# Kernel tuning notes

Measured on AMD Instinct MI355X. Metric: run time of the kernel, lower is better.

Reference implementation:

```python
import math
import jax, jax.numpy as jnp
import numpy as np

B, S, D_MODEL, H = 2, 2048, 1024, 16
HEAD_DIM = D_MODEL // H
NUM_BUCKETS = 32
MAX_DISTANCE = 128
SCALING = HEAD_DIM ** (-0.5)


def setup_inputs() -> dict:
    key = jax.random.key(0)
    ks = jax.random.split(key, 6)
    inp = {
        "hidden_states": jax.random.normal(ks[0], (B, S, D_MODEL), jnp.float32),
        "Wq": jax.random.normal(ks[1], (D_MODEL, D_MODEL), jnp.float32) * (D_MODEL ** -0.5),
        "Wk": jax.random.normal(ks[2], (D_MODEL, D_MODEL), jnp.float32) * (D_MODEL ** -0.5),
        "Wv": jax.random.normal(ks[3], (D_MODEL, D_MODEL), jnp.float32) * (D_MODEL ** -0.5),
        "Wo": jax.random.normal(ks[4], (D_MODEL, D_MODEL), jnp.float32) * (D_MODEL ** -0.5),
        "rel_emb": jax.random.normal(ks[5], (NUM_BUCKETS, H), jnp.float32),
    }
    return inp


def _relative_position_bucket(relative_position, num_buckets=NUM_BUCKETS, max_distance=MAX_DISTANCE):
    # bidirectional (encoder) bucketing, matches T5 _relative_position_bucket
    num_buckets = num_buckets // 2
    relative_buckets = (relative_position > 0).astype(jnp.int32) * num_buckets
    relative_position = jnp.abs(relative_position)
    max_exact = num_buckets // 2
    is_small = relative_position < max_exact
    rp_f = jnp.maximum(relative_position, 1).astype(jnp.float32)  # guard log(0)
    rel_if_large = max_exact + (
        jnp.log(rp_f / max_exact) / math.log(max_distance / max_exact) * (num_buckets - max_exact)
    ).astype(jnp.int32)
    rel_if_large = jnp.minimum(rel_if_large, num_buckets - 1)
    relative_buckets = relative_buckets + jnp.where(is_small, relative_position, rel_if_large)
    return relative_buckets


def compute_bias(rel_emb, q_len, k_len):
    context_position = jnp.arange(q_len)[:, None]
    memory_position = jnp.arange(k_len)[None, :]
    relative_position = memory_position - context_position  # [q, k]
    buckets = _relative_position_bucket(relative_position)
    values = rel_emb[buckets]                  # [q, k, H]
    return jnp.transpose(values, (2, 0, 1))[None]  # [1, H, q, k]


def reference(hidden_states, Wq, Wk, Wv, Wo, rel_emb):
    b, s, _ = hidden_states.shape

    def shape(x):  # [b, s, d_model] -> [b, H, s, head_dim]
        return x.reshape(b, s, H, HEAD_DIM).transpose(0, 2, 1, 3)

    q = shape(hidden_states @ Wq.T)
    k = shape(hidden_states @ Wk.T)
    v = shape(hidden_states @ Wv.T)

    position_bias = compute_bias(rel_emb, s, s)            # [1, H, s, s]
    scores = jnp.einsum("bhqd,bhkd->bhqk", q, k) * SCALING + position_bias
    attn = jax.nn.softmax(scores, axis=-1)
    ctx = jnp.einsum("bhqk,bhkd->bhqd", attn, v)           # [b, H, s, head_dim]
    ctx = ctx.transpose(0, 2, 1, 3).reshape(b, s, D_MODEL)
    return ctx @ Wo.T
```

## Files before the change

### kernel.cpp

```cpp
#include <hip/hip_runtime.h>
#include <math.h>

#define H_    16
#define S_    2048
#define DH_   64
#define DM_   1024
#define NTOK_ 4096
#define NBIAS_ 4095

typedef __attribute__((ext_vector_type(8))) short short8;
typedef __attribute__((ext_vector_type(4))) float f32x4;

#define MFMA16(a, b, c) __builtin_amdgcn_mfma_f32_16x16x32_bf16((a), (b), (c), 0, 0, 0)

__device__ __forceinline__ ushort f2bf(float f) {
  union { float f; unsigned u; } x; x.f = f;
  unsigned r = (x.u + 0x7FFFu + ((x.u >> 16) & 1u)) >> 16;
  return (ushort)r;
}
__device__ __forceinline__ ushort f2bf_fast(float f) {
  union { float f; unsigned u; } x; x.f = f;
  return (ushort)((x.u + 0x8000u) >> 16);
}

__device__ __forceinline__ void ldg16_lds(const ushort* g, ushort* l) {
  __builtin_amdgcn_global_load_lds(
      (const __attribute__((address_space(1))) unsigned int*)g,
      (__attribute__((address_space(3))) unsigned int*)l, 16, 0, 0);
}

__global__ void cast_all_k(const float* __restrict__ hs,
                           const float* __restrict__ wq, const float* __restrict__ wk,
                           const float* __restrict__ wv, const float* __restrict__ wo,
                           ushort* __restrict__ out) {
  int i = (blockIdx.x * blockDim.x + threadIdx.x) * 4;
  const float* src;
  int off;
  if (i < NTOK_ * DM_) {
    src = hs; off = i;
  } else {
    int j = i - NTOK_ * DM_;
    int w = j >> 20;
    off = j & ((DM_ * DM_) - 1);
    src = (w == 0) ? wq : (w == 1) ? wk : (w == 2) ? wv : wo;
  }
  const float4 v = *(const float4*)(src + off);
  ushort4 o;
  o.x = f2bf(v.x); o.y = f2bf(v.y); o.z = f2bf(v.z); o.w = f2bf(v.w);
  *(ushort4*)(out + i) = o;
}

__global__ void build_bias_k(const float* __restrict__ rel_emb, float* __restrict__ biasTab) {
  int d = blockIdx.x * blockDim.x + threadIdx.x;
  if (d >= NBIAS_) return;
  int rp = d - (S_ - 1);
  int ret = (rp > 0) ? 16 : 0;
  int arp = rp < 0 ? -rp : rp;
  int bucket;
  if (arp < 8) {
    bucket = ret + arp;
  } else {
    float t = logf((float)arp * 0.125f);
    t = t / 2.772588722239781f;
    t = t * 8.0f;
    int large = 8 + (int)t;
    if (large > 15) large = 15;
    bucket = ret + large;
  }
  for (int h = 0; h < H_; ++h)
    biasTab[h * NBIAS_ + d] = rel_emb[bucket * H_ + h] * 1.4426950408889634f;
}

__global__ __launch_bounds__(256) void gemm_qkv_k(
    const ushort* __restrict__ X,
    const ushort* __restrict__ Wq, const ushort* __restrict__ Wk, const ushort* __restrict__ Wv,
    ushort* __restrict__ Q, ushort* __restrict__ K, ushort* __restrict__ Vt)
{
  const int z = blockIdx.z;
  const ushort* __restrict__ W = (z == 0) ? Wq : (z == 1) ? Wk : Wv;
  __shared__ __align__(16) ushort As[128 * 32];
  __shared__ __align__(16) ushort Bs[128 * 32];

  const int tid = threadIdx.x;
  const int wave = tid >> 6, lane = tid & 63;
  const int l15 = lane & 15, l4 = lane >> 4;
  const int wm = wave >> 1, wn = wave & 1;
  const int m0 = blockIdx.y * 128;
  const int n0 = blockIdx.x * 128;
  const int srow = lane >> 2, scol = (lane & 3) * 8;

  f32x4 acc[4][4];
#pragma unroll
  for (int mi = 0; mi < 4; ++mi)
#pragma unroll
    for (int ni = 0; ni < 4; ++ni) acc[mi][ni] = (f32x4){0.f, 0.f, 0.f, 0.f};

  for (int k0 = 0; k0 < DM_; k0 += 32) {
    __syncthreads();
#pragma unroll
    for (int i = 0; i < 4; ++i) {
      int c = wave * 4 + i;
      if (c < 8)
        ldg16_lds(X + (size_t)(m0 + c * 16 + srow) * DM_ + k0 + scol, &As[c * 512]);
      else
        ldg16_lds(W + (size_t)(n0 + (c - 8) * 16 + srow) * DM_ + k0 + scol, &Bs[(c - 8) * 512]);
    }
    __syncthreads();
    short8 af[4], bfr[4];
#pragma unroll
    for (int mi = 0; mi < 4; ++mi)
      af[mi] = *(const short8*)&As[(wm * 64 + mi * 16 + l15) * 32 + l4 * 8];
#pragma unroll
    for (int ni = 0; ni < 4; ++ni)
      bfr[ni] = *(const short8*)&Bs[(wn * 64 + ni * 16 + l15) * 32 + l4 * 8];
#pragma unroll
    for (int mi = 0; mi < 4; ++mi)
#pragma unroll
      for (int ni = 0; ni < 4; ++ni)
        acc[mi][ni] = MFMA16(af[mi], bfr[ni], acc[mi][ni]);
  }

#pragma unroll
  for (int mi = 0; mi < 4; ++mi)
#pragma unroll
    for (int ni = 0; ni < 4; ++ni)
#pragma unroll
      for (int r = 0; r < 4; ++r) {
        int m = m0 + wm * 64 + mi * 16 + l4 * 4 + r;
        int n = n0 + wn * 64 + ni * 16 + l15;
        int b = m >> 11, s = m & (S_ - 1);
        int h = n >> 6, d = n & 63;
        ushort bv = f2bf(acc[mi][ni][r]);
        if (z == 0)      Q [((size_t)(b * H_ + h) * S_ + s) * DH_ + d] = bv;
        else if (z == 1) K [((size_t)(b * H_ + h) * S_ + s) * DH_ + d] = bv;
        else             Vt[((size_t)(b * H_ + h) * DH_ + d) * S_ + s] = bv;
      }
}

__global__ __launch_bounds__(256) void gemm_out_k(
    const ushort* __restrict__ A, const ushort* __restrict__ W, float* __restrict__ out)
{
  __shared__ __align__(16) ushort As[128 * 32];
  __shared__ __align__(16) ushort Bs[128 * 32];
  const int tid = threadIdx.x;
  const int wave = tid >> 6, lane = tid & 63;
  const int l15 = lane & 15, l4 = lane >> 4;
  const int wm = wave >> 1, wn = wave & 1;
  const int m0 = blockIdx.y * 128;
  const int n0 = blockIdx.x * 128;
  const int srow = lane >> 2, scol = (lane & 3) * 8;

  f32x4 acc[4][4];
#pragma unroll
  for (int mi = 0; mi < 4; ++mi)
#pragma unroll
    for (int ni = 0; ni < 4; ++ni) acc[mi][ni] = (f32x4){0.f, 0.f, 0.f, 0.f};

  for (int k0 = 0; k0 < DM_; k0 += 32) {
    __syncthreads();
#pragma unroll
    for (int i = 0; i < 4; ++i) {
      int c = wave * 4 + i;
      if (c < 8)
        ldg16_lds(A + (size_t)(m0 + c * 16 + srow) * DM_ + k0 + scol, &As[c * 512]);
      else
        ldg16_lds(W + (size_t)(n0 + (c - 8) * 16 + srow) * DM_ + k0 + scol, &Bs[(c - 8) * 512]);
    }
    __syncthreads();
    short8 af[4], bfr[4];
#pragma unroll
    for (int mi = 0; mi < 4; ++mi)
      af[mi] = *(const short8*)&As[(wm * 64 + mi * 16 + l15) * 32 + l4 * 8];
#pragma unroll
    for (int ni = 0; ni < 4; ++ni)
      bfr[ni] = *(const short8*)&Bs[(wn * 64 + ni * 16 + l15) * 32 + l4 * 8];
#pragma unroll
    for (int mi = 0; mi < 4; ++mi)
#pragma unroll
      for (int ni = 0; ni < 4; ++ni)
        acc[mi][ni] = MFMA16(af[mi], bfr[ni], acc[mi][ni]);
  }

#pragma unroll
  for (int mi = 0; mi < 4; ++mi)
#pragma unroll
    for (int ni = 0; ni < 4; ++ni)
#pragma unroll
      for (int r = 0; r < 4; ++r) {
        int m = m0 + wm * 64 + mi * 16 + l4 * 4 + r;
        int n = n0 + wn * 64 + ni * 16 + l15;
        out[(size_t)m * DM_ + n] = acc[mi][ni][r];
      }
}

__global__ __launch_bounds__(256, 2) void attn_k(
    const ushort* __restrict__ Q, const ushort* __restrict__ K, const ushort* __restrict__ Vt,
    const float* __restrict__ biasTab, ushort* __restrict__ Ctx)
{
  __shared__ __align__(16) ushort Ks[2][2][64][32];
  __shared__ __align__(16) ushort Vs[2][2][64][32];
  __shared__ __align__(16) ushort Ps[4][2][16 * 72];

  const int tid = threadIdx.x;
  const int wave = tid >> 6, lane = tid & 63;
  const int l15 = lane & 15, l4 = lane >> 4;
  const int bh = blockIdx.y;
  const int h = bh & (H_ - 1);
  const int b = bh >> 4;
  const int qb = blockIdx.x * 128;
  const int q0 = qb + wave * 32;
  const int srow = lane >> 2, scol = (lane & 3) * 8;

  const ushort* Qh = Q  + (size_t)bh * S_ * DH_;
  const ushort* Kh = K  + (size_t)bh * S_ * DH_;
  const ushort* Vh = Vt + (size_t)bh * DH_ * S_;

  const float* bpA = biasTab + h * NBIAS_ + 2047 + l15 - (q0 + l4 * 4);

  short8 qfA[2], qfB[2];
#pragma unroll
  for (int kk = 0; kk < 2; ++kk) {
    qfA[kk] = *(const short8*)(Qh + (size_t)(q0 + l15) * DH_ + kk * 32 + l4 * 8);
    qfB[kk] = *(const short8*)(Qh + (size_t)(q0 + 16 + l15) * DH_ + kk * 32 + l4 * 8);
  }

  short8 ones;
#pragma unroll
  for (int i = 0; i < 8; ++i) ones[i] = (short)0x3F80;

  f32x4 ofA[4], ofB[4];
#pragma unroll
  for (int nt = 0; nt < 4; ++nt) { ofA[nt] = (f32x4){0.f,0.f,0.f,0.f}; ofB[nt] = (f32x4){0.f,0.f,0.f,0.f}; }
  f32x4 lsA = (f32x4){0.f,0.f,0.f,0.f}, lsB = (f32x4){0.f,0.f,0.f,0.f};

  ushort* PwA = &Ps[wave][0][0];
  ushort* PwB = &Ps[wave][1][0];

#pragma unroll
  for (int i = 0; i < 2; ++i) {
    int c = wave * 2 + i;
    int kk = c >> 2, rg = c & 3;
    ldg16_lds(Kh + (size_t)(rg * 16 + srow) * DH_ + kk * 32 + scol, &Ks[0][0][0][0] + c * 512);
    ldg16_lds(Vh + (size_t)(rg * 16 + srow) * S_ + kk * 32 + scol, &Vs[0][0][0][0] + c * 512);
  }

  int cur = 0;
  for (int kt = 0; kt < S_; kt += 64) {
    __syncthreads();

    float bA[16], b0[4];
    const float* ptA = bpA + kt;
#pragma unroll
    for (int nt = 0; nt < 4; ++nt)
#pragma unroll
      for (int r = 0; r < 4; ++r)
        bA[nt * 4 + r] = ptA[nt * 16 - r];
#pragma unroll
    for (int r = 0; r < 4; ++r) b0[r] = ptA[-16 - r];

    if (kt + 64 < S_) {
#pragma unroll
      for (int i = 0; i < 2; ++i) {
        int c = wave * 2 + i;
        int kk = c >> 2, rg = c & 3;
        ldg16_lds(Kh + (size_t)(kt + 64 + rg * 16 + srow) * DH_ + kk * 32 + scol,
                  &Ks[cur ^ 1][0][0][0] + c * 512);
        ldg16_lds(Vh + (size_t)(rg * 16 + srow) * S_ + kt + 64 + kk * 32 + scol,
                  &Vs[cur ^ 1][0][0][0] + c * 512);
      }
    }

    f32x4 scA[4], scB[4];
#pragma unroll
    for (int nt = 0; nt < 4; ++nt) { scA[nt] = (f32x4){0.f,0.f,0.f,0.f}; scB[nt] = (f32x4){0.f,0.f,0.f,0.f}; }
#pragma unroll
    for (int kk = 0; kk < 2; ++kk)
#pragma unroll
      for (int nt = 0; nt < 4; ++nt) {
        short8 kf = *(const short8*)&Ks[cur][kk][nt * 16 + l15][l4 * 8];
        scA[nt] = MFMA16(qfA[kk], kf, scA[nt]);
        scB[nt] = MFMA16(qfB[kk], kf, scB[nt]);
      }

#pragma unroll
    for (int nt = 0; nt < 4; ++nt)
#pragma unroll
      for (int r = 0; r < 4; ++r) {
        float p = exp2f(fmaf(scA[nt][r], 0.1803368801f, bA[nt * 4 + r]));
        PwA[(l4 * 4 + r) * 72 + nt * 16 + l15] = f2bf_fast(p);
      }
#pragma unroll
    for (int nt = 0; nt < 4; ++nt)
#pragma unroll
      for (int r = 0; r < 4; ++r) {
        float bb = (nt == 0) ? b0[r] : bA[(nt - 1) * 4 + r];
        float p = exp2f(fmaf(scB[nt][r], 0.1803368801f, bb));
        PwB[(l4 * 4 + r) * 72 + nt * 16 + l15] = f2bf_fast(p);
      }

    short8 pfA[2], pfB[2];
#pragma unroll
    for (int kk = 0; kk < 2; ++kk) {
      pfA[kk] = *(const short8*)&PwA[l15 * 72 + kk * 32 + l4 * 8];
      pfB[kk] = *(const short8*)&PwB[l15 * 72 + kk * 32 + l4 * 8];
    }

#pragma unroll
    for (int kk = 0; kk < 2; ++kk) {
      lsA = MFMA16(pfA[kk], ones, lsA);
      lsB = MFMA16(pfB[kk], ones, lsB);
#pragma unroll
      for (int nt = 0; nt < 4; ++nt) {
        short8 vf = *(const short8*)&Vs[cur][kk][nt * 16 + l15][l4 * 8];
        ofA[nt] = MFMA16(pfA[kk], vf, ofA[nt]);
        ofB[nt] = MFMA16(pfB[kk], vf, ofB[nt]);
      }
    }
    cur ^= 1;
  }

  float invA[4], invB[4];
#pragma unroll
  for (int r = 0; r < 4; ++r) { invA[r] = 1.0f / lsA[r]; invB[r] = 1.0f / lsB[r]; }
#pragma unroll
  for (int nt = 0; nt < 4; ++nt)
#pragma unroll
    for (int r = 0; r < 4; ++r) {
      int tA = b * S_ + q0 + l4 * 4 + r;
      Ctx[(size_t)tA * DM_ + h * 64 + nt * 16 + l15] = f2bf(ofA[nt][r] * invA[r]);
      Ctx[(size_t)(tA + 16) * DM_ + h * 64 + nt * 16 + l15] = f2bf(ofB[nt][r] * invB[r]);
    }
}

extern "C" void kernel_launch(void* const* d_in, const int* in_sizes, int n_in,
                              void* d_out, int out_size, void* d_ws, size_t ws_size,
                              hipStream_t stream) {
  const float* hs  = (const float*)d_in[0];
  const float* Wq  = (const float*)d_in[1];
  const float* Wk  = (const float*)d_in[2];
  const float* Wv  = (const float*)d_in[3];
  const float* Wo  = (const float*)d_in[4];
  const float* rel = (const float*)d_in[5];
  float* out = (float*)d_out;

  ushort* Xb  = (ushort*)d_ws;
  ushort* Wqb = Xb  + (size_t)NTOK_ * DM_;
  ushort* Wkb = Wqb + (size_t)DM_ * DM_;
  ushort* Wvb = Wkb + (size_t)DM_ * DM_;
  ushort* Wob = Wvb + (size_t)DM_ * DM_;
  ushort* Qd  = Wob + (size_t)DM_ * DM_;
  ushort* Kd  = Qd  + (size_t)NTOK_ * DM_;
  ushort* Vtd = Kd  + (size_t)NTOK_ * DM_;
  float* biasTab = (float*)(Vtd + (size_t)NTOK_ * DM_);
  ushort* Ctx = Xb;

  cast_all_k<<<(NTOK_ * DM_ + 4 * DM_ * DM_) / (4 * 256), 256, 0, stream>>>(hs, Wq, Wk, Wv, Wo, Xb);
  build_bias_k<<<16, 256, 0, stream>>>(rel, biasTab);

  gemm_qkv_k<<<dim3(8, 32, 3), 256, 0, stream>>>(Xb, Wqb, Wkb, Wvb, Qd, Kd, Vtd);
  attn_k<<<dim3(S_ / 128, 2 * H_), 256, 0, stream>>>(Qd, Kd, Vtd, biasTab, Ctx);
  gemm_out_k<<<dim3(8, 32), 256, 0, stream>>>(Ctx, Wob, out);
}
```

Before: 221.4 us.

## Fold softmax scale into Q, seed scores with bias, use transposed LDS reads for P

Result: slower. 243.4 us (+9.9%).

```diff
diff --git a/kernel.cpp b/kernel.cpp
--- a/kernel.cpp
+++ b/kernel.cpp
@@ -9,24 +9,31 @@
 #define NBIAS_ 4095
 
 typedef __attribute__((ext_vector_type(8))) short short8;
+typedef __attribute__((ext_vector_type(4))) short s16x4;
 typedef __attribute__((ext_vector_type(4))) float f32x4;
 
 #define MFMA16(a, b, c) __builtin_amdgcn_mfma_f32_16x16x32_bf16((a), (b), (c), 0, 0, 0)
+
+#if __has_builtin(__builtin_amdgcn_exp2f)
+#define EXP2(x) __builtin_amdgcn_exp2f(x)
+#else
+#define EXP2(x) exp2f(x)
+#endif
 
 __device__ __forceinline__ ushort f2bf(float f) {
   union { float f; unsigned u; } x; x.f = f;
   unsigned r = (x.u + 0x7FFFu + ((x.u >> 16) & 1u)) >> 16;
   return (ushort)r;
 }
-__device__ __forceinline__ ushort f2bf_fast(float f) {
-  union { float f; unsigned u; } x; x.f = f;
-  return (ushort)((x.u + 0x8000u) >> 16);
-}
 
 __device__ __forceinline__ void ldg16_lds(const ushort* g, ushort* l) {
   __builtin_amdgcn_global_load_lds(
       (const __attribute__((address_space(1))) unsigned int*)g,
       (__attribute__((address_space(3))) unsigned int*)l, 16, 0, 0);
+}
+
+__device__ __forceinline__ unsigned lds_addr(const void* p) {
+  return (unsigned)(size_t)(const __attribute__((address_space(3))) void*)p;
 }
 
 __global__ void cast_all_k(const float* __restrict__ hs,
@@ -120,6 +127,7 @@
         acc[mi][ni] = MFMA16(af[mi], bfr[ni], acc[mi][ni]);
   }
 
+  const float scl = (z == 0) ? 0.1803368801111137f : 1.0f;
 #pragma unroll
   for (int mi = 0; mi < 4; ++mi)
 #pragma unroll
@@ -130,7 +138,7 @@
         int n = n0 + wn * 64 + ni * 16 + l15;
         int b = m >> 11, s = m & (S_ - 1);
         int h = n >> 6, d = n & 63;
-        ushort bv = f2bf(acc[mi][ni][r]);
+        ushort bv = f2bf(acc[mi][ni][r] * scl);
         if (z == 0)      Q [((size_t)(b * H_ + h) * S_ + s) * DH_ + d] = bv;
         else if (z == 1) K [((size_t)(b * H_ + h) * S_ + s) * DH_ + d] = bv;
         else             Vt[((size_t)(b * H_ + h) * DH_ + d) * S_ + s] = bv;
@@ -199,7 +207,7 @@
 {
   __shared__ __align__(16) ushort Ks[2][2][64][32];
   __shared__ __align__(16) ushort Vs[2][2][64][32];
-  __shared__ __align__(16) ushort Ps[4][2][16 * 72];
+  __shared__ __align__(16) ushort Pt[4][2][64][16];
 
   const int tid = threadIdx.x;
   const int wave = tid >> 6, lane = tid & 63;
@@ -233,8 +241,8 @@
   for (int nt = 0; nt < 4; ++nt) { ofA[nt] = (f32x4){0.f,0.f,0.f,0.f}; ofB[nt] = (f32x4){0.f,0.f,0.f,0.f}; }
   f32x4 lsA = (f32x4){0.f,0.f,0.f,0.f}, lsB = (f32x4){0.f,0.f,0.f,0.f};
 
-  ushort* PwA = &Ps[wave][0][0];
-  ushort* PwB = &Ps[wave][1][0];
+  ushort* PtW = &Pt[wave][0][0][0] + l15 * 16 + l4 * 4;
+  const unsigned trA = lds_addr(&Pt[wave][0][0][0]) + lane * 8;
 
 #pragma unroll
   for (int i = 0; i < 2; ++i) {
@@ -243,20 +251,21 @@
     ldg16_lds(Kh + (size_t)(rg * 16 + srow) * DH_ + kk * 32 + scol, &Ks[0][0][0][0] + c * 512);
     ldg16_lds(Vh + (size_t)(rg * 16 + srow) * S_ + kk * 32 + scol, &Vs[0][0][0][0] + c * 512);
   }
+  float cbX[20], cbY[20];
+  {
+    const float* pt = bpA;
+#pragma unroll
+    for (int nt = 0; nt < 4; ++nt)
+#pragma unroll
+      for (int r = 0; r < 4; ++r) cbX[nt * 4 + r] = pt[nt * 16 - r];
+#pragma unroll
+    for (int r = 0; r < 4; ++r) cbX[16 + r] = pt[-16 - r];
+  }
 
   int cur = 0;
-  for (int kt = 0; kt < S_; kt += 64) {
+
+  auto tile = [&](int kt, float (&cb)[20], float (&nb)[20]) {
     __syncthreads();
-
-    float bA[16], b0[4];
-    const float* ptA = bpA + kt;
-#pragma unroll
-    for (int nt = 0; nt < 4; ++nt)
-#pragma unroll
-      for (int r = 0; r < 4; ++r)
-        bA[nt * 4 + r] = ptA[nt * 16 - r];
-#pragma unroll
-    for (int r = 0; r < 4; ++r) b0[r] = ptA[-16 - r];
 
     if (kt + 64 < S_) {
 #pragma unroll
@@ -268,11 +277,23 @@
         ldg16_lds(Vh + (size_t)(rg * 16 + srow) * S_ + kt + 64 + kk * 32 + scol,
                   &Vs[cur ^ 1][0][0][0] + c * 512);
       }
+      const float* pt = bpA + kt + 64;
+#pragma unroll
+      for (int nt = 0; nt < 4; ++nt)
+#pragma unroll
+        for (int r = 0; r < 4; ++r) nb[nt * 4 + r] = pt[nt * 16 - r];
+#pragma unroll
+      for (int r = 0; r < 4; ++r) nb[16 + r] = pt[-16 - r];
     }
 
     f32x4 scA[4], scB[4];
 #pragma unroll
-    for (int nt = 0; nt < 4; ++nt) { scA[nt] = (f32x4){0.f,0.f,0.f,0.f}; scB[nt] = (f32x4){0.f,0.f,0.f,0.f}; }
+    for (int nt = 0; nt < 4; ++nt) {
+      scA[nt] = (f32x4){cb[nt * 4 + 0], cb[nt * 4 + 1], cb[nt * 4 + 2], cb[nt * 4 + 3]};
+      if (nt == 0) scB[0] = (f32x4){cb[16], cb[17], cb[18], cb[19]};
+      else scB[nt] = (f32x4){cb[(nt - 1) * 4 + 0], cb[(nt - 1) * 4 + 1],
+                             cb[(nt - 1) * 4 + 2], cb[(nt - 1) * 4 + 3]};
+    }
 #pragma unroll
     for (int kk = 0; kk < 2; ++kk)
 #pragma unroll
@@ -283,40 +304,63 @@
       }
 
 #pragma unroll
-    for (int nt = 0; nt < 4; ++nt)
-#pragma unroll
-      for (int r = 0; r < 4; ++r) {
-        float p = exp2f(fmaf(scA[nt][r], 0.1803368801f, bA[nt * 4 + r]));
-        PwA[(l4 * 4 + r) * 72 + nt * 16 + l15] = f2bf_fast(p);
-      }
-#pragma unroll
-    for (int nt = 0; nt < 4; ++nt)
-#pragma unroll
-      for (int r = 0; r < 4; ++r) {
-        float bb = (nt == 0) ? b0[r] : bA[(nt - 1) * 4 + r];
-        float p = exp2f(fmaf(scB[nt][r], 0.1803368801f, bb));
-        PwB[(l4 * 4 + r) * 72 + nt * 16 + l15] = f2bf_fast(p);
-      }
-
+    for (int nt = 0; nt < 4; ++nt) {
+      unsigned w0, w1;
+      {
+        float e0 = EXP2(scA[nt][0]), e1 = EXP2(scA[nt][1]);
+        float e2 = EXP2(scA[nt][2]), e3 = EXP2(scA[nt][3]);
+        asm("v_cvt_pk_bf16_f32 %0, %1, %2" : "=v"(w0) : "v"(e0), "v"(e1));
+        asm("v_cvt_pk_bf16_f32 %0, %1, %2" : "=v"(w1) : "v"(e2), "v"(e3));
+        *(uint2*)(PtW + nt * 256) = make_uint2(w0, w1);
+      }
+      {
+        float e0 = EXP2(scB[nt][0]), e1 = EXP2(scB[nt][1]);
+        float e2 = EXP2(scB[nt][2]), e3 = EXP2(scB[nt][3]);
+        asm("v_cvt_pk_bf16_f32 %0, %1, %2" : "=v"(w0) : "v"(e0), "v"(e1));
+        asm("v_cvt_pk_bf16_f32 %0, %1, %2" : "=v"(w1) : "v"(e2), "v"(e3));
+        *(uint2*)(PtW + 1024 + nt * 256) = make_uint2(w0, w1);
+      }
+    }
+
+    asm volatile("" ::: "memory");
+    s16x4 t0, t1, t2, t3, t4, t5, t6, t7;
+    asm volatile("ds_read_b64_tr_b16 %0, %1 offset:0"    : "=v"(t0) : "v"(trA));
+    asm volatile("ds_read_b64_tr_b16 %0, %1 offset:512"  : "=v"(t1) : "v"(trA));
+    asm volatile("ds_read_b64_tr_b16 %0, %1 offset:1024" : "=v"(t2) : "v"(trA));
+    asm volatile("ds_read_b64_tr_b16 %0, %1 offset:1536" : "=v"(t3) : "v"(trA));
+    asm volatile("ds_read_b64_tr_b16 %0, %1 offset:2048" : "=v"(t4) : "v"(trA));
+    asm volatile("ds_read_b64_tr_b16 %0, %1 offset:2560" : "=v"(t5) : "v"(trA));
+    asm volatile("ds_read_b64_tr_b16 %0, %1 offset:3072" : "=v"(t6) : "v"(trA));
+    asm volatile("ds_read_b64_tr_b16 %0, %1 offset:3584" : "=v"(t7) : "v"(trA));
+    asm volatile("s_waitcnt lgkmcnt(0)" ::: "memory");
+    __builtin_amdgcn_sched_barrier(0);
     short8 pfA[2], pfB[2];
-#pragma unroll
-    for (int kk = 0; kk < 2; ++kk) {
-      pfA[kk] = *(const short8*)&PwA[l15 * 72 + kk * 32 + l4 * 8];
-      pfB[kk] = *(const short8*)&PwB[l15 * 72 + kk * 32 + l4 * 8];
-    }
-
+    pfA[0] = __builtin_shufflevector(t0, t1, 0, 1, 2, 3, 4, 5, 6, 7);
+    pfA[1] = __builtin_shufflevector(t2, t3, 0, 1, 2, 3, 4, 5, 6, 7);
+    pfB[0] = __builtin_shufflevector(t4, t5, 0, 1, 2, 3, 4, 5, 6, 7);
+    pfB[1] = __builtin_shufflevector(t6, t7, 0, 1, 2, 3, 4, 5, 6, 7);
+
+    const ushort* Vb = &Vs[cur][0][0][0];
 #pragma unroll
     for (int kk = 0; kk < 2; ++kk) {
       lsA = MFMA16(pfA[kk], ones, lsA);
       lsB = MFMA16(pfB[kk], ones, lsB);
 #pragma unroll
       for (int nt = 0; nt < 4; ++nt) {
-        short8 vf = *(const short8*)&Vs[cur][kk][nt * 16 + l15][l4 * 8];
+        const ushort* vp = Vb + (kk * 64 + nt * 16 + l15) * 32 + l4 * 4;
+        s16x4 v0 = *(const s16x4*)vp;
+        s16x4 v1 = *(const s16x4*)(vp + 16);
+        short8 vf = __builtin_shufflevector(v0, v1, 0, 1, 2, 3, 4, 5, 6, 7);
         ofA[nt] = MFMA16(pfA[kk], vf, ofA[nt]);
         ofB[nt] = MFMA16(pfB[kk], vf, ofB[nt]);
       }
     }
     cur ^= 1;
+  };
+
+  for (int kt = 0; kt < S_; kt += 128) {
+    tile(kt, cbX, cbY);
+    tile(kt + 64, cbY, cbX);
   }
 
   float invA[4], invB[4];
```

## Prefetch bias one tile ahead, fold Q scaling into projection, use raw exp2

Applied to the files above, without the earlier changes.

Result: faster. 207.0 us (-6.5%).

```diff
diff --git a/kernel.cpp b/kernel.cpp
--- a/kernel.cpp
+++ b/kernel.cpp
@@ -12,6 +12,12 @@
 typedef __attribute__((ext_vector_type(4))) float f32x4;
 
 #define MFMA16(a, b, c) __builtin_amdgcn_mfma_f32_16x16x32_bf16((a), (b), (c), 0, 0, 0)
+
+#if __has_builtin(__builtin_amdgcn_exp2f)
+#define EXP2(x) __builtin_amdgcn_exp2f(x)
+#else
+#define EXP2(x) exp2f(x)
+#endif
 
 __device__ __forceinline__ ushort f2bf(float f) {
   union { float f; unsigned u; } x; x.f = f;
@@ -120,6 +126,7 @@
         acc[mi][ni] = MFMA16(af[mi], bfr[ni], acc[mi][ni]);
   }
 
+  const float scl = (z == 0) ? 0.1803368801111137f : 1.0f;
 #pragma unroll
   for (int mi = 0; mi < 4; ++mi)
 #pragma unroll
@@ -130,7 +137,7 @@
         int n = n0 + wn * 64 + ni * 16 + l15;
         int b = m >> 11, s = m & (S_ - 1);
         int h = n >> 6, d = n & 63;
-        ushort bv = f2bf(acc[mi][ni][r]);
+        ushort bv = f2bf(acc[mi][ni][r] * scl);
         if (z == 0)      Q [((size_t)(b * H_ + h) * S_ + s) * DH_ + d] = bv;
         else if (z == 1) K [((size_t)(b * H_ + h) * S_ + s) * DH_ + d] = bv;
         else             Vt[((size_t)(b * H_ + h) * DH_ + d) * S_ + s] = bv;
@@ -243,20 +250,21 @@
     ldg16_lds(Kh + (size_t)(rg * 16 + srow) * DH_ + kk * 32 + scol, &Ks[0][0][0][0] + c * 512);
     ldg16_lds(Vh + (size_t)(rg * 16 + srow) * S_ + kk * 32 + scol, &Vs[0][0][0][0] + c * 512);
   }
+  float cbX[20], cbY[20];
+  {
+    const float* pt = bpA;
+#pragma unroll
+    for (int nt = 0; nt < 4; ++nt)
+#pragma unroll
+      for (int r = 0; r < 4; ++r) cbX[nt * 4 + r] = pt[nt * 16 - r];
+#pragma unroll
+    for (int r = 0; r < 4; ++r) cbX[16 + r] = pt[-16 - r];
+  }
 
   int cur = 0;
-  for (int kt = 0; kt < S_; kt += 64) {
-    __syncthreads();
-
-    float bA[16], b0[4];
-    const float* ptA = bpA + kt;
-#pragma unroll
-    for (int nt = 0; nt < 4; ++nt)
-#pragma unroll
-      for (int r = 0; r < 4; ++r)
-        bA[nt * 4 + r] = ptA[nt * 16 - r];
-#pragma unroll
-    for (int r = 0; r < 4; ++r) b0[r] = ptA[-16 - r];
+
+  auto tile = [&](int kt, float (&cb)[20], float (&nb)[20]) {
+    __syncthreads();
 
     if (kt + 64 < S_) {
 #pragma unroll
@@ -268,11 +276,24 @@
         ldg16_lds(Vh + (size_t)(rg * 16 + srow) * S_ + kt + 64 + kk * 32 + scol,
                   &Vs[cur ^ 1][0][0][0] + c * 512);
       }
+      const float* pt = bpA + kt + 64;
+#pragma unroll
+      for (int nt = 0; nt < 4; ++nt)
+#pragma unroll
+        for (int r = 0; r < 4; ++r) nb[nt * 4 + r] = pt[nt * 16 - r];
+#pragma unroll
+      for (int r = 0; r < 4; ++r) nb[16 + r] = pt[-16 - r];
     }
 
     f32x4 scA[4], scB[4];
 #pragma unroll
-    for (int nt = 0; nt < 4; ++nt) { scA[nt] = (f32x4){0.f,0.f,0.f,0.f}; scB[nt] = (f32x4){0.f,0.f,0.f,0.f}; }
+    for (int nt = 0; nt < 4; ++nt) {
+      scA[nt] = (f32x4){cb[nt * 4 + 0], cb[nt * 4 + 1], cb[nt * 4 + 2], cb[nt * 4 + 3]};
+      if (nt == 0) scB[0] = (f32x4){cb[16], cb[17], cb[18], cb[19]};
+      else scB[nt] = (f32x4){cb[(nt - 1) * 4 + 0], cb[(nt - 1) * 4 + 1],
+                             cb[(nt - 1) * 4 + 2], cb[(nt - 1) * 4 + 3]};
+    }
+    __builtin_amdgcn_s_setprio(1);
 #pragma unroll
     for (int kk = 0; kk < 2; ++kk)
 #pragma unroll
@@ -281,21 +302,14 @@
         scA[nt] = MFMA16(qfA[kk], kf, scA[nt]);
         scB[nt] = MFMA16(qfB[kk], kf, scB[nt]);
       }
+    __builtin_amdgcn_s_setprio(0);
 
 #pragma unroll
     for (int nt = 0; nt < 4; ++nt)
 #pragma unroll
       for (int r = 0; r < 4; ++r) {
-        float p = exp2f(fmaf(scA[nt][r], 0.1803368801f, bA[nt * 4 + r]));
-        PwA[(l4 * 4 + r) * 72 + nt * 16 + l15] = f2bf_fast(p);
-      }
-#pragma unroll
-    for (int nt = 0; nt < 4; ++nt)
-#pragma unroll
-      for (int r = 0; r < 4; ++r) {
-        float bb = (nt == 0) ? b0[r] : bA[(nt - 1) * 4 + r];
-        float p = exp2f(fmaf(scB[nt][r], 0.1803368801f, bb));
-        PwB[(l4 * 4 + r) * 72 + nt * 16 + l15] = f2bf_fast(p);
+        PwA[(l4 * 4 + r) * 72 + nt * 16 + l15] = f2bf_fast(EXP2(scA[nt][r]));
+        PwB[(l4 * 4 + r) * 72 + nt * 16 + l15] = f2bf_fast(EXP2(scB[nt][r]));
       }
 
     short8 pfA[2], pfB[2];
@@ -305,6 +319,7 @@
       pfB[kk] = *(const short8*)&PwB[l15 * 72 + kk * 32 + l4 * 8];
     }
 
+    __builtin_amdgcn_s_setprio(1);
 #pragma unroll
     for (int kk = 0; kk < 2; ++kk) {
       lsA = MFMA16(pfA[kk], ones, lsA);
@@ -316,7 +331,13 @@
         ofB[nt] = MFMA16(pfB[kk], vf, ofB[nt]);
       }
     }
+    __builtin_amdgcn_s_setprio(0);
     cur ^= 1;
+  };
+
+  for (int kt = 0; kt < S_; kt += 128) {
+    tile(kt, cbX, cbY);
+    tile(kt + 64, cbY, cbX);
   }
 
   float invA[4], invB[4];
```
